# Performance work log

Measured on AMD Instinct MI355X. Metric: run time of the kernel, lower is better.

Reference implementation:

```python
import jax, jax.numpy as jnp
import numpy as np

N_NODES = 18870
HIDDEN = 256
K = 20
HEAD_HIDDEN = 512
N_CLASSES = 3
N_GENES_OUT = 6640
B = 1024
FALLBACK_SCALE = 1e-3
LN_EPS = 1e-5


def setup_inputs() -> dict:
    key = jax.random.key(0)
    ks = jax.random.split(key, 8)
    node_idx = jax.random.randint(ks[0], (B,), 0, N_NODES)
    topk_neighbors = jax.random.randint(ks[1], (N_NODES, K), 0, N_NODES)
    node_emb = jax.random.normal(ks[2], (N_NODES, HIDDEN), dtype=jnp.float32)
    fallback_emb = jax.random.normal(ks[3], (HIDDEN,), dtype=jnp.float32) * 0.02
    w_attn = jax.random.normal(ks[4], (HIDDEN,), dtype=jnp.float32) * 0.02
    ln_gamma = jnp.ones((2 * HIDDEN,), dtype=jnp.float32)
    ln_beta = jnp.zeros((2 * HIDDEN,), dtype=jnp.float32)
    W1 = jax.random.normal(ks[5], (2 * HIDDEN, HEAD_HIDDEN), dtype=jnp.float32) * 0.02
    b1 = jnp.zeros((HEAD_HIDDEN,), dtype=jnp.float32)
    W2 = jax.random.normal(ks[6], (HEAD_HIDDEN, N_CLASSES * N_GENES_OUT), dtype=jnp.float32) * 0.02
    b2 = jnp.zeros((N_CLASSES * N_GENES_OUT,), dtype=jnp.float32)
    return dict(node_idx=node_idx, topk_neighbors=topk_neighbors, node_emb=node_emb,
                fallback_emb=fallback_emb, w_attn=w_attn, ln_gamma=ln_gamma, ln_beta=ln_beta,
                W1=W1, b1=b1, W2=W2, b2=b2)


def reference(node_idx, topk_neighbors, node_emb, fallback_emb, w_attn,
              ln_gamma, ln_beta, W1, b1, W2, b2):
    valid = node_idx >= 0                                   # [B]
    safe_idx = jnp.where(valid, node_idx, 0)                # [B]
    graph_emb = node_emb[safe_idx]                          # [B, H]
    pert_emb = jnp.where(valid[:, None],
                         graph_emb + FALLBACK_SCALE * fallback_emb[None, :],
                         fallback_emb[None, :])              # [B, H]

    nbr_idx = topk_neighbors[safe_idx]                      # [B, K]
    valid_nbr = nbr_idx >= 0                                # [B, K]
    nbr_emb = node_emb[jnp.clip(nbr_idx, 0)]                # [B, K, H]
    nbr_emb = nbr_emb * valid_nbr[..., None].astype(nbr_emb.dtype)

    # Faithful to the original broadcast: scores[b,k] = pert_emb[b,0] * (nbr_emb[b,k] . w_attn)
    scores = pert_emb[:, 0:1] * jnp.einsum('bkh,h->bk', nbr_emb, w_attn)  # [B, K]
    scores = jnp.where(valid_nbr, scores, -1e9)
    has_valid = jnp.any(valid_nbr, axis=1, keepdims=True)   # [B, 1]
    attn = jnp.where(has_valid, jax.nn.softmax(scores, axis=-1),
                     jnp.zeros_like(scores))                # [B, K]
    context = jnp.einsum('bk,bkh->bh', attn, nbr_emb)       # [B, H]

    combined = jnp.concatenate([pert_emb, context], axis=-1)  # [B, 2H]
    mu = jnp.mean(combined, axis=-1, keepdims=True)
    var = jnp.mean(jnp.square(combined - mu), axis=-1, keepdims=True)
    x = (combined - mu) * jax.lax.rsqrt(var + LN_EPS) * ln_gamma + ln_beta
    h = jax.nn.gelu(x @ W1 + b1, approximate=False)          # [B, HH]
    logits = h @ W2 + b2                                     # [B, 3*6640]
    return logits.reshape(-1, N_CLASSES, N_GENES_OUT)


if __name__ == '__main__':
    out = reference(**setup_inputs())
    print(out.shape)
```

## Files before the change

kernel.cpp:

```cpp
#include <hip/hip_runtime.h>
#include <hip/hip_bf16.h>
#include <math.h>

#define HIDDEN 256
#define K_NBR 20
#define NB 1024

typedef __bf16 bf16x8 __attribute__((ext_vector_type(8)));
typedef float f32x4 __attribute__((ext_vector_type(4)));

__device__ __forceinline__ float wave_sum(float v) {
#pragma unroll
    for (int o = 32; o > 0; o >>= 1) v += __shfl_xor(v, o, 64);
    return v;
}

__device__ __forceinline__ void gload16(const void* g, void* l) {
    __builtin_amdgcn_global_load_lds(
        (const __attribute__((address_space(1))) void*)g,
        (__attribute__((address_space(3))) void*)l, 16, 0, 0);
}

__device__ __forceinline__ int swz_chunk(int g, int row) {
    return (g & ~7) | ((g & 7) ^ (row & 7));
}

__device__ __forceinline__ void attn_ln_body(
    int b, int t, const int* __restrict__ node_idx, const int* __restrict__ topk,
    const float* __restrict__ node_emb, const float* __restrict__ fallback,
    const float* __restrict__ w_attn, const float* __restrict__ gamma,
    const float* __restrict__ beta, __bf16* __restrict__ xb, int swz_on,
    float* pe, float (*nbr)[HIDDEN], int* nidx, float* sc, float* red)
{
    int lane = t & 63, w = t >> 6;

    int nid = node_idx[b];
    bool valid = nid >= 0;
    int safe = valid ? nid : 0;

    pe[t] = valid ? node_emb[(size_t)safe * HIDDEN + t] + 1e-3f * fallback[t]
                  : fallback[t];
    if (t < K_NBR) nidx[t] = topk[safe * K_NBR + t];
    __syncthreads();

    for (int r = 0; r < K_NBR; ++r) {
        int gi = nidx[r];
        nbr[r][t] = (gi >= 0) ? node_emb[(size_t)gi * HIDDEN + t] : 0.f;
    }
    __syncthreads();

    float pe0 = pe[0];
    float wa[4];
#pragma unroll
    for (int q = 0; q < 4; ++q) wa[q] = w_attn[lane + 64 * q];
    for (int k = w; k < K_NBR; k += 4) {
        float p = 0.f;
#pragma unroll
        for (int q = 0; q < 4; ++q) p += nbr[k][lane + 64 * q] * wa[q];
        p = wave_sum(p);
        if (lane == 0) sc[k] = (nidx[k] >= 0) ? pe0 * p : -1e9f;
    }
    __syncthreads();

    bool has_valid = false;
#pragma unroll
    for (int k = 0; k < K_NBR; ++k) has_valid |= (nidx[k] >= 0);
    float mx = -1e30f;
#pragma unroll
    for (int k = 0; k < K_NBR; ++k) mx = fmaxf(mx, sc[k]);
    float at[K_NBR];
    float s = 0.f;
#pragma unroll
    for (int k = 0; k < K_NBR; ++k) { at[k] = expf(sc[k] - mx); s += at[k]; }
    float inv = has_valid ? 1.f / s : 0.f;

    float ctx = 0.f;
#pragma unroll
    for (int k = 0; k < K_NBR; ++k) ctx += (at[k] * inv) * nbr[k][t];

    float v0 = pe[t], v1 = ctx;
    float s1 = wave_sum(v0 + v1);
    float s2 = wave_sum(v0 * v0 + v1 * v1);
    if (lane == 0) { red[w] = s1; red[4 + w] = s2; }
    __syncthreads();
    s1 = red[0] + red[1] + red[2] + red[3];
    s2 = red[4] + red[5] + red[6] + red[7];
    float mu = s1 / 512.f;
    float var = s2 / 512.f - mu * mu;
    float rs = rsqrtf(var + 1e-5f);

    size_t base = (size_t)b * 512;
    int mask = swz_on ? (b & 7) : 0;
    {
        int e = t;
        int g = e >> 3, off = e & 7;
        int gp = (g & ~7) | ((g & 7) ^ mask);
        xb[base + gp * 8 + off] = (__bf16)((v0 - mu) * rs * gamma[t] + beta[t]);
        e = 256 + t;
        g = e >> 3;
        gp = (g & ~7) | ((g & 7) ^ mask);
        xb[base + gp * 8 + off] = (__bf16)((v1 - mu) * rs * gamma[256 + t] + beta[256 + t]);
    }
}

__device__ __forceinline__ void transpose_body(
    const float* __restrict__ Wm, __bf16* __restrict__ WT,
    int Kd, int Nd, int Np, int bx, int by, int t)
{
    int n = bx * 64 + (t >> 2);
    int k0 = by * 32 + (t & 3) * 8;
    bool ok = n < Nd;
    bf16x8 v;
#pragma unroll
    for (int j = 0; j < 8; ++j) {
        float f = ok ? Wm[(size_t)(k0 + j) * Nd + n] : 0.f;
        v[j] = (__bf16)f;
    }
    if (n < Np) {
        int gp = swz_chunk(k0 >> 3, n);
        *(bf16x8*)(WT + (size_t)n * Kd + gp * 8) = v;
    }
}

__global__ __launch_bounds__(256) void prep_kernel(
    const int* __restrict__ node_idx, const int* __restrict__ topk,
    const float* __restrict__ node_emb, const float* __restrict__ fallback,
    const float* __restrict__ w_attn, const float* __restrict__ gamma,
    const float* __restrict__ beta, const float* __restrict__ W1,
    const float* __restrict__ W2, __bf16* __restrict__ xb,
    __bf16* __restrict__ w1t, __bf16* __restrict__ w2t)
{
    __shared__ float pe[HIDDEN];
    __shared__ float nbr[K_NBR][HIDDEN];
    __shared__ int   nidx[K_NBR];
    __shared__ float sc[K_NBR];
    __shared__ float red[8];

    int bid = blockIdx.x;
    int t = threadIdx.x;
    if (bid < 4992) {
        transpose_body(W2, w2t, 512, 19920, 19968, bid % 312, bid / 312, t);
        return;
    }
    bid -= 4992;
    if (bid < 128) {
        transpose_body(W1, w1t, 512, 512, 512, bid % 8, bid / 8, t);
        return;
    }
    bid -= 128;
    attn_ln_body(bid, t, node_idx, topk, node_emb, fallback, w_attn, gamma, beta,
                 xb, 1, pe, nbr, nidx, sc, red);
}

__global__ __launch_bounds__(256) void attn_ln_kernel(
    const int* __restrict__ node_idx, const int* __restrict__ topk,
    const float* __restrict__ node_emb, const float* __restrict__ fallback,
    const float* __restrict__ w_attn, const float* __restrict__ gamma,
    const float* __restrict__ beta, __bf16* __restrict__ xb, int swz_on)
{
    __shared__ float pe[HIDDEN];
    __shared__ float nbr[K_NBR][HIDDEN];
    __shared__ int   nidx[K_NBR];
    __shared__ float sc[K_NBR];
    __shared__ float red[8];
    attn_ln_body(blockIdx.x, threadIdx.x, node_idx, topk, node_emb, fallback,
                 w_attn, gamma, beta, xb, swz_on, pe, nbr, nidx, sc, red);
}

__global__ __launch_bounds__(256, 4) void gemm1_kernel(
    const __bf16* __restrict__ A, const __bf16* __restrict__ BT,
    const float* __restrict__ bias, __bf16* __restrict__ Cb,
    int M, int N, int K)
{
    constexpr int BK = 64;
    __shared__ __bf16 As[2][64 * BK];
    __shared__ __bf16 Bs[2][64 * BK];

    int t = threadIdx.x;
    int lane = t & 63;
    int wid = t >> 6;
    int wm = wid >> 1, wn = wid & 1;
    int lo = lane & 15, hi = lane >> 4;

    int nwg = gridDim.x;
    int bid = blockIdx.x;
    int cpx = nwg >> 3;
    int lid = (bid & 7) * cpx + (bid >> 3);
    int m0 = (lid & 15) * 64;
    int n0 = (lid >> 4) * 64;

    int rsub = lane >> 3, kc = lane & 7;

    auto STAGE = [&](int buf, int k0) {
#pragma unroll
        for (int j = 0; j < 2; ++j) {
            int rb = j * 32 + wid * 8;
            gload16(A + (size_t)(m0 + rb + rsub) * K + k0 + kc * 8, &As[buf][rb * BK]);
        }
#pragma unroll
        for (int j = 0; j < 2; ++j) {
            int rb = j * 32 + wid * 8;
            gload16(BT + (size_t)(n0 + rb + rsub) * K + k0 + kc * 8, &Bs[buf][rb * BK]);
        }
    };

    f32x4 acc[2][2];
#pragma unroll
    for (int m = 0; m < 2; ++m)
#pragma unroll
        for (int n = 0; n < 2; ++n)
            acc[m][n] = (f32x4){0.f, 0.f, 0.f, 0.f};

    auto COMPUTE = [&](int buf) {
#pragma unroll
        for (int ks = 0; ks < 2; ++ks) {
            bf16x8 af[2], bfr[2];
#pragma unroll
            for (int m = 0; m < 2; ++m) {
                int r = wm * 32 + m * 16 + lo;
                af[m] = *(const bf16x8*)&As[buf][r * BK + (((ks * 4 + hi) ^ (r & 7)) * 8)];
            }
#pragma unroll
            for (int n = 0; n < 2; ++n) {
                int r = wn * 32 + n * 16 + lo;
                bfr[n] = *(const bf16x8*)&Bs[buf][r * BK + (((ks * 4 + hi) ^ (r & 7)) * 8)];
            }
#pragma unroll
            for (int m = 0; m < 2; ++m)
#pragma unroll
                for (int n = 0; n < 2; ++n)
                    acc[m][n] = __builtin_amdgcn_mfma_f32_16x16x32_bf16(
                        af[m], bfr[n], acc[m][n], 0, 0, 0);
        }
    };

    const int nt = K / BK;
    STAGE(0, 0);
    __syncthreads();
    for (int tt = 0; tt < nt; ++tt) {
        if (tt + 1 < nt) STAGE((tt + 1) & 1, (tt + 1) * BK);
        COMPUTE(tt & 1);
        __syncthreads();
    }

#pragma unroll
    for (int m = 0; m < 2; ++m) {
        int gr = m0 + wm * 32 + m * 16 + hi * 4;
#pragma unroll
        for (int n = 0; n < 2; ++n) {
            int gc = n0 + wn * 32 + n * 16 + lo;
            float bv = bias[gc];
#pragma unroll
            for (int r = 0; r < 4; ++r) {
                float v = acc[m][n][r] + bv;
                float g = v * 0.5f * (1.f + erff(v * 0.70710678118f));
                int row = gr + r;
                int gp = swz_chunk(gc >> 3, row);
                Cb[(size_t)row * N + gp * 8 + (gc & 7)] = (__bf16)g;
            }
        }
    }
}

__global__ __launch_bounds__(512, 4) void gemm2_kernel(
    const __bf16* __restrict__ A, const __bf16* __restrict__ BT,
    const float* __restrict__ bias, float* __restrict__ C,
    int M, int N, int K)
{
    constexpr int BK = 64;
    __shared__ __bf16 As[2][128 * BK];
    __shared__ __bf16 Bs[2][128 * BK];

    int t = threadIdx.x;
    int lane = t & 63;
    int wid = t >> 6;
    int wm = wid >> 2, wn = wid & 3;
    int lo = lane & 15, hi = lane >> 4;

    int nwg = gridDim.x;
    int bid = blockIdx.x;
    int cpx = nwg >> 3;
    int lid = (bid & 7) * cpx + (bid >> 3);
    int m0 = (lid & 7) * 128;
    int n0 = (lid >> 3) * 128;

    int rsub = lane >> 3, kc = lane & 7;

    auto STAGE = [&](int buf, int k0) {
#pragma unroll
        for (int j = 0; j < 2; ++j) {
            int rb = j * 64 + wid * 8;
            gload16(A + (size_t)(m0 + rb + rsub) * K + k0 + kc * 8, &As[buf][rb * BK]);
        }
#pragma unroll
        for (int j = 0; j < 2; ++j) {
            int rb = j * 64 + wid * 8;
            gload16(BT + (size_t)(n0 + rb + rsub) * K + k0 + kc * 8, &Bs[buf][rb * BK]);
        }
    };

    f32x4 acc[4][2];
#pragma unroll
    for (int m = 0; m < 4; ++m)
#pragma unroll
        for (int n = 0; n < 2; ++n)
            acc[m][n] = (f32x4){0.f, 0.f, 0.f, 0.f};

    auto COMPUTE = [&](int buf) {
#pragma unroll
        for (int ks = 0; ks < 2; ++ks) {
            bf16x8 af[4], bfr[2];
#pragma unroll
            for (int m = 0; m < 4; ++m) {
                int r = wm * 64 + m * 16 + lo;
                af[m] = *(const bf16x8*)&As[buf][r * BK + (((ks * 4 + hi) ^ (r & 7)) * 8)];
            }
#pragma unroll
            for (int n = 0; n < 2; ++n) {
                int r = wn * 32 + n * 16 + lo;
                bfr[n] = *(const bf16x8*)&Bs[buf][r * BK + (((ks * 4 + hi) ^ (r & 7)) * 8)];
            }
#pragma unroll
            for (int m = 0; m < 4; ++m)
#pragma unroll
                for (int n = 0; n < 2; ++n)
                    acc[m][n] = __builtin_amdgcn_mfma_f32_16x16x32_bf16(
                        af[m], bfr[n], acc[m][n], 0, 0, 0);
        }
    };

    const int nt = K / BK;
    STAGE(0, 0);
    __syncthreads();
    for (int tt = 0; tt < nt; ++tt) {
        if (tt + 1 < nt) STAGE((tt + 1) & 1, (tt + 1) * BK);
        COMPUTE(tt & 1);
        __syncthreads();
    }

#pragma unroll
    for (int m = 0; m < 4; ++m) {
        int gr = m0 + wm * 64 + m * 16 + hi * 4;
#pragma unroll
        for (int n = 0; n < 2; ++n) {
            int gc = n0 + wn * 32 + n * 16 + lo;
            if (gc < N) {
                float bv = bias[gc];
#pragma unroll
                for (int r = 0; r < 4; ++r)
                    C[(size_t)(gr + r) * N + gc] = acc[m][n][r] + bv;
            }
        }
    }
}

template<bool GELU>
__global__ __launch_bounds__(256) void gemm_kernel(
    const __bf16* __restrict__ A, const float* __restrict__ Bm,
    const float* __restrict__ bias, float* __restrict__ Cf, __bf16* __restrict__ Cb,
    int M, int N, int K)
{
    constexpr int BK = 64;
    __shared__ bf16x8 As[2][128 * 8];
    __shared__ bf16x8 Bs[2][128 * 8];

    int t = threadIdx.x;
    int lane = t & 63;
    int wid = t >> 6;
    int wm = wid >> 1, wn = wid & 1;
    int lo = lane & 15, hi = lane >> 4;

    int n0 = blockIdx.x * 128;
    int m0 = blockIdx.y * 128;

    int cA = t & 7;
    int rA = t >> 3;
    int nl = t & 127;
    int kcb = t >> 7;

    bf16x8 a_st[4];
    bf16x8 b_st[4];

    auto LOAD = [&](int k0) {
#pragma unroll
        for (int i = 0; i < 4; ++i)
            a_st[i] = *(const bf16x8*)(A + (size_t)(m0 + rA + 32 * i) * K + k0 + cA * 8);
        int col = n0 + nl;
        bool ok = col < N;
#pragma unroll
        for (int i = 0; i < 4; ++i) {
            int kcv = kcb + 2 * i;
            bf16x8 v;
#pragma unroll
            for (int j = 0; j < 8; ++j) {
                float f = ok ? Bm[(size_t)(k0 + kcv * 8 + j) * N + col] : 0.f;
                v[j] = (__bf16)f;
            }
            b_st[i] = v;
        }
    };
    auto WRITE = [&](int buf) {
#pragma unroll
        for (int i = 0; i < 4; ++i) {
            int r = rA + 32 * i;
            As[buf][r * 8 + (cA ^ (r & 7))] = a_st[i];
        }
#pragma unroll
        for (int i = 0; i < 4; ++i) {
            int kcv = kcb + 2 * i;
            Bs[buf][nl * 8 + (kcv ^ (nl & 7))] = b_st[i];
        }
    };

    f32x4 acc[4][4];
#pragma unroll
    for (int m = 0; m < 4; ++m)
#pragma unroll
        for (int n = 0; n < 4; ++n)
            acc[m][n] = (f32x4){0.f, 0.f, 0.f, 0.f};

    auto COMPUTE = [&](int buf) {
#pragma unroll
        for (int ks = 0; ks < 2; ++ks) {
            bf16x8 af[4], bfr[4];
#pragma unroll
            for (int m = 0; m < 4; ++m) {
                int r = wm * 64 + m * 16 + lo;
                af[m] = As[buf][r * 8 + ((ks * 4 + hi) ^ (r & 7))];
            }
#pragma unroll
            for (int n = 0; n < 4; ++n) {
                int r = wn * 64 + n * 16 + lo;
                bfr[n] = Bs[buf][r * 8 + ((ks * 4 + hi) ^ (r & 7))];
            }
#pragma unroll
            for (int m = 0; m < 4; ++m)
#pragma unroll
                for (int n = 0; n < 4; ++n)
                    acc[m][n] = __builtin_amdgcn_mfma_f32_16x16x32_bf16(
                        af[m], bfr[n], acc[m][n], 0, 0, 0);
        }
    };

    const int nt = K / BK;
    LOAD(0);
    WRITE(0);
    __syncthreads();
    for (int tt = 0; tt < nt; ++tt) {
        int cur = tt & 1;
        if (tt + 1 < nt) LOAD((tt + 1) * BK);
        COMPUTE(cur);
        if (tt + 1 < nt) WRITE(cur ^ 1);
        __syncthreads();
    }

#pragma unroll
    for (int m = 0; m < 4; ++m) {
        int gr = m0 + wm * 64 + m * 16 + hi * 4;
#pragma unroll
        for (int n = 0; n < 4; ++n) {
            int gc = n0 + wn * 64 + n * 16 + lo;
            if (gc < N) {
                float bv = bias[gc];
#pragma unroll
                for (int r = 0; r < 4; ++r) {
                    float v = acc[m][n][r] + bv;
                    if constexpr (GELU) {
                        float g = v * 0.5f * (1.f + erff(v * 0.70710678118f));
                        Cb[(size_t)(gr + r) * N + gc] = (__bf16)g;
                    } else {
                        Cf[(size_t)(gr + r) * N + gc] = v;
                    }
                }
            }
        }
    }
}

extern "C" void kernel_launch(void* const* d_in, const int* in_sizes, int n_in,
                              void* d_out, int out_size, void* d_ws, size_t ws_size,
                              hipStream_t stream) {
    const int*   node_idx = (const int*)d_in[0];
    const int*   topk     = (const int*)d_in[1];
    const float* node_emb = (const float*)d_in[2];
    const float* fallback = (const float*)d_in[3];
    const float* w_attn   = (const float*)d_in[4];
    const float* gamma    = (const float*)d_in[5];
    const float* beta     = (const float*)d_in[6];
    const float* W1       = (const float*)d_in[7];
    const float* b1       = (const float*)d_in[8];
    const float* W2       = (const float*)d_in[9];
    const float* b2       = (const float*)d_in[10];
    float* out = (float*)d_out;

    const int M = 1024, Kd = 512, N1 = 512, N2 = 19920;
    const int N2p = 19968;

    __bf16* xb  = (__bf16*)d_ws;
    __bf16* h   = xb + (size_t)M * Kd;
    __bf16* w1t = h + (size_t)M * Kd;
    __bf16* w2t = w1t + (size_t)N1 * Kd;
    size_t needed = ((size_t)2 * M * Kd + (size_t)N1 * Kd + (size_t)N2p * Kd) * sizeof(__bf16);

    if (ws_size >= needed) {
        prep_kernel<<<4992 + 128 + 1024, 256, 0, stream>>>(
            node_idx, topk, node_emb, fallback, w_attn, gamma, beta, W1, W2,
            xb, w1t, w2t);

        gemm1_kernel<<<dim3(128), 256, 0, stream>>>(
            xb, w1t, b1, h, M, N1, Kd);

        gemm2_kernel<<<dim3(1248), 512, 0, stream>>>(
            h, w2t, b2, out, M, N2, Kd);
    } else {
        attn_ln_kernel<<<NB, 256, 0, stream>>>(node_idx, topk, node_emb, fallback,
                                               w_attn, gamma, beta, xb, 0);
        gemm_kernel<true><<<dim3(4, 8), 256, 0, stream>>>(
            xb, W1, b1, nullptr, h, M, N1, Kd);
        gemm_kernel<false><<<dim3(156, 8), 256, 0, stream>>>(
            h, W2, b2, out, nullptr, M, N2, Kd);
    }
}
```

Measured before the change: 75.06 us.

## Deepen gemm2 pipeline to four-stage BK=32 ring with finer waitcnt barriers

Rewrites the W2 GEMM main loop to use a 4-buffer LDS ring with BK=32. It prefetches three tiles ahead and uses explicit vmcnt/lgkmcnt waits with raw s_barrier instead of __syncthreads. The LDS swizzle changes to a 2-bit XOR pattern to match the 64-byte rows, and the W2 transpose and GEMM1 output layouts are updated to match. It also raises wave priority around the MFMA block. The aim is to hide global-to-LDS latency behind MFMA work, at the cost of fragile hand-tuned wait counts and twice as many loop iterations.

```diff
diff --git a/kernel.cpp b/kernel.cpp
--- a/kernel.cpp
+++ b/kernel.cpp
@@ -21,8 +21,11 @@
         (__attribute__((address_space(3))) void*)l, 16, 0, 0);
 }
 
-__device__ __forceinline__ int swz_chunk(int g, int row) {
+__device__ __forceinline__ int swz3(int g, int row) {
     return (g & ~7) | ((g & 7) ^ (row & 7));
+}
+__device__ __forceinline__ int swz2(int g, int row) {
+    return (g & ~3) | ((g & 3) ^ ((row >> 1) & 3));
 }
 
 __device__ __forceinline__ void attn_ln_body(
@@ -105,7 +108,7 @@
 
 __device__ __forceinline__ void transpose_body(
     const float* __restrict__ Wm, __bf16* __restrict__ WT,
-    int Kd, int Nd, int Np, int bx, int by, int t)
+    int Kd, int Nd, int Np, int bx, int by, int t, int two_bit)
 {
     int n = bx * 64 + (t >> 2);
     int k0 = by * 32 + (t & 3) * 8;
@@ -117,7 +120,8 @@
         v[j] = (__bf16)f;
     }
     if (n < Np) {
-        int gp = swz_chunk(k0 >> 3, n);
+        int g = k0 >> 3;
+        int gp = two_bit ? swz2(g, n) : swz3(g, n);
         *(bf16x8*)(WT + (size_t)n * Kd + gp * 8) = v;
     }
 }
@@ -139,12 +143,12 @@
     int bid = blockIdx.x;
     int t = threadIdx.x;
     if (bid < 4992) {
-        transpose_body(W2, w2t, 512, 19920, 19968, bid % 312, bid / 312, t);
+        transpose_body(W2, w2t, 512, 19920, 19968, bid % 312, bid / 312, t, 1);
         return;
     }
     bid -= 4992;
     if (bid < 128) {
-        transpose_body(W1, w1t, 512, 512, 512, bid % 8, bid / 8, t);
+        transpose_body(W1, w1t, 512, 512, 512, bid % 8, bid / 8, t, 0);
         return;
     }
     bid -= 128;
@@ -255,7 +259,7 @@
                 float v = acc[m][n][r] + bv;
                 float g = v * 0.5f * (1.f + erff(v * 0.70710678118f));
                 int row = gr + r;
-                int gp = swz_chunk(gc >> 3, row);
+                int gp = swz2(gc >> 3, row);
                 Cb[(size_t)row * N + gp * 8 + (gc & 7)] = (__bf16)g;
             }
         }
@@ -267,9 +271,9 @@
     const float* __restrict__ bias, float* __restrict__ C,
     int M, int N, int K)
 {
-    constexpr int BK = 64;
-    __shared__ __bf16 As[2][128 * BK];
-    __shared__ __bf16 Bs[2][128 * BK];
+    constexpr int BK = 32;
+    __shared__ __bf16 As[4][128 * BK];
+    __shared__ __bf16 Bs[4][128 * BK];
 
     int t = threadIdx.x;
     int lane = t & 63;
@@ -284,19 +288,15 @@
     int m0 = (lid & 7) * 128;
     int n0 = (lid >> 3) * 128;
 
-    int rsub = lane >> 3, kc = lane & 7;
-
-    auto STAGE = [&](int buf, int k0) {
-#pragma unroll
-        for (int j = 0; j < 2; ++j) {
-            int rb = j * 64 + wid * 8;
-            gload16(A + (size_t)(m0 + rb + rsub) * K + k0 + kc * 8, &As[buf][rb * BK]);
-        }
-#pragma unroll
-        for (int j = 0; j < 2; ++j) {
-            int rb = j * 64 + wid * 8;
-            gload16(BT + (size_t)(n0 + rb + rsub) * K + k0 + kc * 8, &Bs[buf][rb * BK]);
-        }
+    int srow = wid * 16 + (lane >> 2);
+    int ssl = lane & 3;
+
+    const int nt = K / BK;
+
+    auto STAGE = [&](int buf, int tt) {
+        int k0 = tt * BK;
+        gload16(A + (size_t)(m0 + srow) * K + k0 + ssl * 8, &As[buf][wid * 512]);
+        gload16(BT + (size_t)(n0 + srow) * K + k0 + ssl * 8, &Bs[buf][wid * 512]);
     };
 
     f32x4 acc[4][2];
@@ -307,35 +307,64 @@
             acc[m][n] = (f32x4){0.f, 0.f, 0.f, 0.f};
 
     auto COMPUTE = [&](int buf) {
-#pragma unroll
-        for (int ks = 0; ks < 2; ++ks) {
-            bf16x8 af[4], bfr[2];
-#pragma unroll
-            for (int m = 0; m < 4; ++m) {
-                int r = wm * 64 + m * 16 + lo;
-                af[m] = *(const bf16x8*)&As[buf][r * BK + (((ks * 4 + hi) ^ (r & 7)) * 8)];
-            }
-#pragma unroll
-            for (int n = 0; n < 2; ++n) {
-                int r = wn * 32 + n * 16 + lo;
-                bfr[n] = *(const bf16x8*)&Bs[buf][r * BK + (((ks * 4 + hi) ^ (r & 7)) * 8)];
-            }
-#pragma unroll
-            for (int m = 0; m < 4; ++m)
-#pragma unroll
-                for (int n = 0; n < 2; ++n)
-                    acc[m][n] = __builtin_amdgcn_mfma_f32_16x16x32_bf16(
-                        af[m], bfr[n], acc[m][n], 0, 0, 0);
-        }
-    };
-
-    const int nt = K / BK;
+        bf16x8 af[4], bfr[2];
+#pragma unroll
+        for (int m = 0; m < 4; ++m) {
+            int r = wm * 64 + m * 16 + lo;
+            int ph = hi ^ ((r >> 1) & 3);
+            af[m] = *(const bf16x8*)&As[buf][r * BK + ph * 8];
+        }
+#pragma unroll
+        for (int n = 0; n < 2; ++n) {
+            int r = wn * 32 + n * 16 + lo;
+            int ph = hi ^ ((r >> 1) & 3);
+            bfr[n] = *(const bf16x8*)&Bs[buf][r * BK + ph * 8];
+        }
+        __builtin_amdgcn_s_setprio(1);
+#pragma unroll
+        for (int m = 0; m < 4; ++m)
+#pragma unroll
+            for (int n = 0; n < 2; ++n)
+                acc[m][n] = __builtin_amdgcn_mfma_f32_16x16x32_bf16(
+                    af[m], bfr[n], acc[m][n], 0, 0, 0);
+        __builtin_amdgcn_s_setprio(0);
+    };
+
     STAGE(0, 0);
-    __syncthreads();
-    for (int tt = 0; tt < nt; ++tt) {
-        if (tt + 1 < nt) STAGE((tt + 1) & 1, (tt + 1) * BK);
-        COMPUTE(tt & 1);
-        __syncthreads();
+    STAGE(1, 1);
+    STAGE(2, 2);
+
+    for (int tt = 0; tt < nt - 3; ++tt) {
+        asm volatile("s_waitcnt lgkmcnt(0)" ::: "memory");
+        __builtin_amdgcn_sched_barrier(0);
+        __builtin_amdgcn_s_barrier();
+        STAGE((tt + 3) & 3, tt + 3);
+        asm volatile("s_waitcnt vmcnt(6)" ::: "memory");
+        __builtin_amdgcn_sched_barrier(0);
+        __builtin_amdgcn_s_barrier();
+        __builtin_amdgcn_sched_barrier(0);
+        COMPUTE(tt & 3);
+    }
+    {
+        asm volatile("s_waitcnt vmcnt(4) lgkmcnt(0)" ::: "memory");
+        __builtin_amdgcn_sched_barrier(0);
+        __builtin_amdgcn_s_barrier();
+        __builtin_amdgcn_sched_barrier(0);
+        COMPUTE((nt - 3) & 3);
+    }
+    {
+        asm volatile("s_waitcnt vmcnt(2) lgkmcnt(0)" ::: "memory");
+        __builtin_amdgcn_sched_barrier(0);
+        __builtin_amdgcn_s_barrier();
+        __builtin_amdgcn_sched_barrier(0);
+        COMPUTE((nt - 2) & 3);
+    }
+    {
+        asm volatile("s_waitcnt vmcnt(0) lgkmcnt(0)" ::: "memory");
+        __builtin_amdgcn_sched_barrier(0);
+        __builtin_amdgcn_s_barrier();
+        __builtin_amdgcn_sched_barrier(0);
+        COMPUTE((nt - 1) & 3);
     }
 
 #pragma unroll
```

Result: slower. 77.05 us (+2.7%).

## Widen gemm2 tile to 128x256 with BK=32 and 2-bit LDS swizzle

Applied to the files above, without the earlier changes.

The output GEMM now uses 128x256 tiles with a K step of 32, giving each wave a 64x64 sub-tile (4x4 MFMAs) and halving the grid to 624 workgroups. The swizzle on the transposed W2 and on the hidden activations changes to a 2-bit XOR pattern to match the 32-wide K chunks in LDS. The W2 transpose loads become nontemporal. The aim is more operand reuse per LDS load and fewer blocks. The cost is more accumulator registers, more barriers per K, and fewer workgroups to fill the CUs.

```diff
diff --git a/kernel.cpp b/kernel.cpp
--- a/kernel.cpp
+++ b/kernel.cpp
@@ -21,8 +21,11 @@
         (__attribute__((address_space(3))) void*)l, 16, 0, 0);
 }
 
-__device__ __forceinline__ int swz_chunk(int g, int row) {
+__device__ __forceinline__ int swz3(int g, int row) {
     return (g & ~7) | ((g & 7) ^ (row & 7));
+}
+__device__ __forceinline__ int swz2(int g, int row) {
+    return (g & ~3) | ((g & 3) ^ ((row >> 1) & 3));
 }
 
 __device__ __forceinline__ void attn_ln_body(
@@ -105,7 +108,7 @@
 
 __device__ __forceinline__ void transpose_body(
     const float* __restrict__ Wm, __bf16* __restrict__ WT,
-    int Kd, int Nd, int Np, int bx, int by, int t)
+    int Kd, int Nd, int Np, int bx, int by, int t, int two_bit)
 {
     int n = bx * 64 + (t >> 2);
     int k0 = by * 32 + (t & 3) * 8;
@@ -113,11 +116,12 @@
     bf16x8 v;
 #pragma unroll
     for (int j = 0; j < 8; ++j) {
-        float f = ok ? Wm[(size_t)(k0 + j) * Nd + n] : 0.f;
+        float f = ok ? __builtin_nontemporal_load(&Wm[(size_t)(k0 + j) * Nd + n]) : 0.f;
         v[j] = (__bf16)f;
     }
     if (n < Np) {
-        int gp = swz_chunk(k0 >> 3, n);
+        int g = k0 >> 3;
+        int gp = two_bit ? swz2(g, n) : swz3(g, n);
         *(bf16x8*)(WT + (size_t)n * Kd + gp * 8) = v;
     }
 }
@@ -139,12 +143,12 @@
     int bid = blockIdx.x;
     int t = threadIdx.x;
     if (bid < 4992) {
-        transpose_body(W2, w2t, 512, 19920, 19968, bid % 312, bid / 312, t);
+        transpose_body(W2, w2t, 512, 19920, 19968, bid % 312, bid / 312, t, 1);
         return;
     }
     bid -= 4992;
     if (bid < 128) {
-        transpose_body(W1, w1t, 512, 512, 512, bid % 8, bid / 8, t);
+        transpose_body(W1, w1t, 512, 512, 512, bid % 8, bid / 8, t, 0);
         return;
     }
     bid -= 128;
@@ -255,7 +259,7 @@
                 float v = acc[m][n][r] + bv;
                 float g = v * 0.5f * (1.f + erff(v * 0.70710678118f));
                 int row = gr + r;
-                int gp = swz_chunk(gc >> 3, row);
+                int gp = swz2(gc >> 3, row);
                 Cb[(size_t)row * N + gp * 8 + (gc & 7)] = (__bf16)g;
             }
         }
@@ -267,9 +271,9 @@
     const float* __restrict__ bias, float* __restrict__ C,
     int M, int N, int K)
 {
-    constexpr int BK = 64;
+    constexpr int BK = 32;
     __shared__ __bf16 As[2][128 * BK];
-    __shared__ __bf16 Bs[2][128 * BK];
+    __shared__ __bf16 Bs[2][256 * BK];
 
     int t = threadIdx.x;
     int lane = t & 63;
@@ -282,58 +286,50 @@
     int cpx = nwg >> 3;
     int lid = (bid & 7) * cpx + (bid >> 3);
     int m0 = (lid & 7) * 128;
-    int n0 = (lid >> 3) * 128;
-
-    int rsub = lane >> 3, kc = lane & 7;
-
-    auto STAGE = [&](int buf, int k0) {
-#pragma unroll
-        for (int j = 0; j < 2; ++j) {
-            int rb = j * 64 + wid * 8;
-            gload16(A + (size_t)(m0 + rb + rsub) * K + k0 + kc * 8, &As[buf][rb * BK]);
-        }
-#pragma unroll
-        for (int j = 0; j < 2; ++j) {
-            int rb = j * 64 + wid * 8;
-            gload16(BT + (size_t)(n0 + rb + rsub) * K + k0 + kc * 8, &Bs[buf][rb * BK]);
-        }
-    };
-
-    f32x4 acc[4][2];
+    int n0 = (lid >> 3) * 256;
+
+    int srow = t >> 2;
+    int ssl = t & 3;
+
+    auto STAGE = [&](int buf, int tt) {
+        int k0 = tt * BK;
+        gload16(A + (size_t)(m0 + srow) * K + k0 + ssl * 8, &As[buf][wid * 512]);
+        gload16(BT + (size_t)(n0 + srow) * K + k0 + ssl * 8, &Bs[buf][wid * 512]);
+        gload16(BT + (size_t)(n0 + 128 + srow) * K + k0 + ssl * 8, &Bs[buf][4096 + wid * 512]);
+    };
+
+    f32x4 acc[4][4];
 #pragma unroll
     for (int m = 0; m < 4; ++m)
 #pragma unroll
-        for (int n = 0; n < 2; ++n)
+        for (int n = 0; n < 4; ++n)
             acc[m][n] = (f32x4){0.f, 0.f, 0.f, 0.f};
 
     auto COMPUTE = [&](int buf) {
-#pragma unroll
-        for (int ks = 0; ks < 2; ++ks) {
-            bf16x8 af[4], bfr[2];
-#pragma unroll
-            for (int m = 0; m < 4; ++m) {
-                int r = wm * 64 + m * 16 + lo;
-                af[m] = *(const bf16x8*)&As[buf][r * BK + (((ks * 4 + hi) ^ (r & 7)) * 8)];
-            }
-#pragma unroll
-            for (int n = 0; n < 2; ++n) {
-                int r = wn * 32 + n * 16 + lo;
-                bfr[n] = *(const bf16x8*)&Bs[buf][r * BK + (((ks * 4 + hi) ^ (r & 7)) * 8)];
-            }
-#pragma unroll
-            for (int m = 0; m < 4; ++m)
-#pragma unroll
-                for (int n = 0; n < 2; ++n)
-                    acc[m][n] = __builtin_amdgcn_mfma_f32_16x16x32_bf16(
-                        af[m], bfr[n], acc[m][n], 0, 0, 0);
-        }
+        bf16x8 af[4], bfr[4];
+#pragma unroll
+        for (int m = 0; m < 4; ++m) {
+            int r = wm * 64 + m * 16 + lo;
+            af[m] = *(const bf16x8*)&As[buf][r * BK + ((hi ^ ((r >> 1) & 3)) * 8)];
+        }
+#pragma unroll
+        for (int n = 0; n < 4; ++n) {
+            int r = wn * 64 + n * 16 + lo;
+            bfr[n] = *(const bf16x8*)&Bs[buf][r * BK + ((hi ^ ((r >> 1) & 3)) * 8)];
+        }
+#pragma unroll
+        for (int m = 0; m < 4; ++m)
+#pragma unroll
+            for (int n = 0; n < 4; ++n)
+                acc[m][n] = __builtin_amdgcn_mfma_f32_16x16x32_bf16(
+                    af[m], bfr[n], acc[m][n], 0, 0, 0);
     };
 
     const int nt = K / BK;
     STAGE(0, 0);
     __syncthreads();
     for (int tt = 0; tt < nt; ++tt) {
-        if (tt + 1 < nt) STAGE((tt + 1) & 1, (tt + 1) * BK);
+        if (tt + 1 < nt) STAGE((tt + 1) & 1, tt + 1);
         COMPUTE(tt & 1);
         __syncthreads();
     }
@@ -342,8 +338,8 @@
     for (int m = 0; m < 4; ++m) {
         int gr = m0 + wm * 64 + m * 16 + hi * 4;
 #pragma unroll
-        for (int n = 0; n < 2; ++n) {
-            int gc = n0 + wn * 32 + n * 16 + lo;
+        for (int n = 0; n < 4; ++n) {
+            int gc = n0 + wn * 64 + n * 16 + lo;
             if (gc < N) {
                 float bv = bias[gc];
 #pragma unroll
@@ -510,7 +506,7 @@
         gemm1_kernel<<<dim3(128), 256, 0, stream>>>(
             xb, w1t, b1, h, M, N1, Kd);
 
-        gemm2_kernel<<<dim3(1248), 512, 0, stream>>>(
+        gemm2_kernel<<<dim3(624), 512, 0, stream>>>(
             h, w2t, b2, out, M, N2, Kd);
     } else {
         attn_ln_kernel<<<NB, 256, 0, stream>>>(node_idx, topk, node_emb, fallback,
```

After: 86.48 us. +15.2%, slower.
